# Kernel optimization log

Measured on AMD Instinct MI355X. Metric: run time of the kernel, lower is better.

The kernel has to match this reference:

```python
import jax, jax.numpy as jnp
import numpy as np

B, S, D, H = 4, 1024, 1024, 16
HD = D // H
EPS = 1e-5


def _layernorm(x, g, b):
    m = jnp.mean(x, axis=-1, keepdims=True)
    v = jnp.mean((x - m) ** 2, axis=-1, keepdims=True)
    return (x - m) * jax.lax.rsqrt(v + EPS) * g + b


def setup_inputs() -> dict:
    key = jax.random.key(0)
    ks = jax.random.split(key, 8)
    sc = 1.0 / np.sqrt(D)
    return {
        "x": jax.random.normal(ks[0], (B, S, D), dtype=jnp.float32),
        "seq_len": jax.random.randint(ks[1], (B,), 1, S + 1, dtype=jnp.int32),
        "Wq": jax.random.normal(ks[2], (D, D), dtype=jnp.float32) * sc,
        "bq": jnp.zeros((D,), dtype=jnp.float32),
        "Wk": jax.random.normal(ks[3], (D, D), dtype=jnp.float32) * sc,
        "bk": jnp.zeros((D,), dtype=jnp.float32),
        "Wv": jax.random.normal(ks[4], (D, D), dtype=jnp.float32) * sc,
        "bv": jnp.zeros((D,), dtype=jnp.float32),
        "ln_g": jnp.ones((HD,), dtype=jnp.float32),
        "ln_b": jnp.zeros((HD,), dtype=jnp.float32),
    }


def reference(x, seq_len, Wq, bq, Wk, bk, Wv, bv, ln_g, ln_b):
    # Faithful quirk: k and v are projections of the ALREADY projected q.
    q = x @ Wq.T + bq                      # [B,S,D]
    k = q @ Wk.T + bk
    v = q @ Wv.T + bv
    # [B,S,D] -> [B,H,S,HD]
    def split_heads(t):
        return t.reshape(B, S, H, HD).transpose(0, 2, 1, 3)
    q, k, v = split_heads(q), split_heads(k), split_heads(v)
    # shared per-head LayerNorm over head_dim
    q = _layernorm(q, ln_g, ln_b)
    k = _layernorm(k, ln_g, ln_b)
    v = _layernorm(v, ln_g, ln_b)
    # raw scores (no temperature scaling in the original; temperature=1.0 unused)
    scores = jnp.einsum("bhqd,bhkd->bhqk", q, k)
    # encoder_mask: multiplicative validity mask on key positions, repeated per head
    mask = (jnp.arange(S)[None, :] < seq_len[:, None]).astype(scores.dtype)  # [B,S]
    scores = scores * mask[:, None, None, :]
    attn = jax.nn.softmax(scores, axis=-1)
    # dropout is identity at inference
    out = jnp.einsum("bhqk,bhkd->bhqd", attn, v)
    return out.transpose(0, 2, 1, 3).reshape(B, S, D)
```

## Files before the change

kernel.cpp:

```cpp
#include <hip/hip_runtime.h>

#define B_  4
#define S_  1024
#define D_  1024
#define H_  16
#define HD_ 64
#define EPS_ 1e-5f

typedef _Float16 f16x8 __attribute__((ext_vector_type(8)));
typedef _Float16 f16x4 __attribute__((ext_vector_type(4)));
typedef __bf16 bf16x8 __attribute__((ext_vector_type(8)));
typedef float  f32x4  __attribute__((ext_vector_type(4)));
typedef unsigned short ushort4v __attribute__((ext_vector_type(4)));

#define GLD16(gp, lp) __builtin_amdgcn_global_load_lds( \
    (const __attribute__((address_space(1))) void*)(gp), \
    (__attribute__((address_space(3))) void*)(lp), 16, 0, 0)

static __device__ __forceinline__ unsigned pk2bf(float a, float b) {
  union { __bf16 h; unsigned short u; } ua, ub;
  ua.h = (__bf16)a; ub.h = (__bf16)b;
  return (unsigned)ua.u | ((unsigned)ub.u << 16);
}

__global__ __launch_bounds__(256) void cvt_all(
    const float* __restrict__ x,  _Float16* __restrict__ xh,
    const float* __restrict__ Wq, _Float16* __restrict__ wqh,
    const float* __restrict__ Wk, _Float16* __restrict__ wkh,
    const float* __restrict__ Wv, _Float16* __restrict__ wvh,
    float* __restrict__ Vtail) {
  int bid = blockIdx.x;
  if (bid >= 7168) {
    int i = (bid - 7168) * 1024 + threadIdx.x * 4;
    *(float4*)(Vtail + i) = make_float4(0.f, 0.f, 0.f, 0.f);
    return;
  }
  const float* src; _Float16* dst; int base;
  if (bid < 4096)      { src = x;  dst = xh;  base = bid; }
  else if (bid < 5120) { src = Wq; dst = wqh; base = bid - 4096; }
  else if (bid < 6144) { src = Wk; dst = wkh; base = bid - 5120; }
  else                 { src = Wv; dst = wvh; base = bid - 6144; }
  int i = base * 1024 + threadIdx.x * 4;
  float4 f = *(const float4*)(src + i);
  f16x4 h;
  h.x = (_Float16)f.x; h.y = (_Float16)f.y; h.z = (_Float16)f.z; h.w = (_Float16)f.w;
  *(f16x4*)(dst + i) = h;
}

__global__ __launch_bounds__(256, 2) void gemm_q_ln(
    const _Float16* __restrict__ A,
    const _Float16* __restrict__ Bw,
    const float* __restrict__ bias,
    const float* __restrict__ ln_g, const float* __restrict__ ln_b,
    _Float16* __restrict__ qh,
    _Float16* __restrict__ Qn)
{
  __shared__ _Float16 As[4 * 128 * 32];
  __shared__ _Float16 Bs[4 * 64 * 32];

  int tid  = threadIdx.x;
  int lane = tid & 63;
  int wave = tid >> 6;
  int qd = lane >> 4, l15 = lane & 15;

  int flat = blockIdx.x + 16 * blockIdx.y;
  int swz  = (flat & 7) * 64 + (flat >> 3);
  int bx = swz & 15, by = swz >> 4;

  long row0 = (long)by * 128;
  long col0 = (long)bx * 64;

  int r_a = tid >> 2;
  int c_a = (tid & 3) * 8;

  f32x4 acc[2][4] = {};

  for (int kk = 0; kk < D_; kk += 128) {
    for (int ks2 = 0; ks2 < 4; ks2++) {
      GLD16(A  + (row0 + r_a) * D_ + kk + ks2 * 32 + c_a,      As + ks2 * 4096 + tid * 8);
      GLD16(A  + (row0 + 64 + r_a) * D_ + kk + ks2 * 32 + c_a, As + ks2 * 4096 + 2048 + tid * 8);
      GLD16(Bw + (col0 + r_a) * D_ + kk + ks2 * 32 + c_a,      Bs + ks2 * 2048 + tid * 8);
    }
    __syncthreads();

    for (int ks = 0; ks < 4; ks++) {
      f16x8 af[2], bfr[4];
      for (int i = 0; i < 2; i++)
        af[i]  = *(const f16x8*)(As + ks * 4096 + (wave * 32 + i * 16 + l15) * 32 + qd * 8);
      for (int j = 0; j < 4; j++)
        bfr[j] = *(const f16x8*)(Bs + ks * 2048 + (j * 16 + l15) * 32 + qd * 8);
      for (int i = 0; i < 2; i++)
        for (int j = 0; j < 4; j++)
          acc[i][j] = __builtin_amdgcn_mfma_f32_16x16x32_f16(af[i], bfr[j], acc[i][j], 0, 0, 0);
    }
    __syncthreads();
  }

  int h = bx;
  long rw = row0 + wave * 32;
  int bb = (int)(rw >> 10);
  long bh = (long)bb * H_ + h;
  float gv[4], bl[4], bc[4];
  for (int j = 0; j < 4; j++) {
    int d = j * 16 + l15;
    gv[j] = ln_g[d]; bl[j] = ln_b[d]; bc[j] = bias[h * 64 + d];
  }
  for (int i = 0; i < 2; i++) {
    float m4[4], i4[4];
    for (int r = 0; r < 4; r++) {
      float s = 0.f, q = 0.f;
      for (int j = 0; j < 4; j++) {
        float y = acc[i][j][r] + bc[j];
        s += y; q = fmaf(y, y, q);
      }
      for (int off = 1; off < 16; off <<= 1) {
        s += __shfl_xor(s, off, 64);
        q += __shfl_xor(q, off, 64);
      }
      float m = s * (1.f / 64.f);
      m4[r] = m;
      i4[r] = rsqrtf(q * (1.f / 64.f) - m * m + EPS_);
    }
    for (int r = 0; r < 4; r++) {
      long srow = rw + i * 16 + qd * 4 + r;
      long sloc = srow & (S_ - 1);
      for (int j = 0; j < 4; j++) {
        float y = acc[i][j][r] + bc[j];
        qh[srow * D_ + h * 64 + j * 16 + l15] = (_Float16)y;
        Qn[(bh * S_ + sloc) * HD_ + j * 16 + l15] =
            (_Float16)((y - m4[r]) * i4[r] * gv[j] + bl[j]);
      }
    }
  }
}

__global__ __launch_bounds__(256, 2) void gemm_kv_ln(
    const _Float16* __restrict__ A,
    const _Float16* __restrict__ Bk, const float* __restrict__ bk,
    const _Float16* __restrict__ Bv, const float* __restrict__ bv,
    const float* __restrict__ ln_g, const float* __restrict__ ln_b,
    const int* __restrict__ seq_len,
    _Float16* __restrict__ Kn,
    unsigned short* __restrict__ Vt,
    float* __restrict__ Vtail)
{
  __shared__ _Float16 As[4 * 128 * 32];
  __shared__ _Float16 Bs[4 * 128 * 32];

  int tid  = threadIdx.x;
  int lane = tid & 63;
  int wave = tid >> 6;
  int wm = wave >> 1, wn = wave & 1;
  int qd = lane >> 4, l15 = lane & 15;

  int flat = blockIdx.x + 8 * blockIdx.y + 256 * blockIdx.z;
  int swz  = (flat & 7) * 64 + (flat >> 3);
  int z    = swz >> 8;
  int rem  = swz & 255;
  int by   = rem >> 3, bx = rem & 7;

  const _Float16* Bm = z ? Bv : Bk;
  const float* bias  = z ? bv : bk;

  long row0 = (long)by * 128;
  long col0 = (long)bx * 128;

  int r_a = tid >> 2;
  int c_a = (tid & 3) * 8;

  f32x4 acc[4][4] = {};

  for (int kk = 0; kk < D_; kk += 128) {
    for (int ks2 = 0; ks2 < 4; ks2++) {
      GLD16(A  + (row0 + r_a) * D_ + kk + ks2 * 32 + c_a,      As + ks2 * 4096 + tid * 8);
      GLD16(A  + (row0 + 64 + r_a) * D_ + kk + ks2 * 32 + c_a, As + ks2 * 4096 + 2048 + tid * 8);
      GLD16(Bm + (col0 + r_a) * D_ + kk + ks2 * 32 + c_a,      Bs + ks2 * 4096 + tid * 8);
      GLD16(Bm + (col0 + 64 + r_a) * D_ + kk + ks2 * 32 + c_a, Bs + ks2 * 4096 + 2048 + tid * 8);
    }
    __syncthreads();

    for (int ks = 0; ks < 4; ks++) {
      f16x8 af[4], bfr[4];
      for (int t = 0; t < 4; t++) {
        af[t]  = *(const f16x8*)(As + ks * 4096 + (wm * 64 + t * 16 + l15) * 32 + qd * 8);
        bfr[t] = *(const f16x8*)(Bs + ks * 4096 + (wn * 64 + t * 16 + l15) * 32 + qd * 8);
      }
      for (int i = 0; i < 4; i++)
        for (int j = 0; j < 4; j++)
          acc[i][j] = __builtin_amdgcn_mfma_f32_16x16x32_f16(af[i], bfr[j], acc[i][j], 0, 0, 0);
    }
    __syncthreads();
  }

  int h = bx * 2 + wn;
  long rw = row0 + wm * 64;
  int bb = (int)(rw >> 10);
  long bh = (long)bb * H_ + h;
  float gv[4], bl[4], bc[4];
  for (int j = 0; j < 4; j++) {
    int d = j * 16 + l15;
    gv[j] = ln_g[d]; bl[j] = ln_b[d]; bc[j] = bias[h * 64 + d];
  }

  if (z == 0) {
    for (int i = 0; i < 4; i++) {
      float m4[4], i4[4];
      for (int r = 0; r < 4; r++) {
        float s = 0.f, q = 0.f;
        for (int j = 0; j < 4; j++) {
          float y = acc[i][j][r] + bc[j];
          s += y; q = fmaf(y, y, q);
        }
        for (int off = 1; off < 16; off <<= 1) {
          s += __shfl_xor(s, off, 64);
          q += __shfl_xor(q, off, 64);
        }
        float m = s * (1.f / 64.f);
        m4[r] = m;
        i4[r] = rsqrtf(q * (1.f / 64.f) - m * m + EPS_);
      }
      for (int r = 0; r < 4; r++) {
        long sloc = (rw + i * 16 + qd * 4 + r) & (S_ - 1);
        for (int j = 0; j < 4; j++) {
          float y = acc[i][j][r] + bc[j];
          Kn[(bh * S_ + sloc) * HD_ + j * 16 + l15] =
              (_Float16)((y - m4[r]) * i4[r] * gv[j] + bl[j]);
        }
      }
    }
  } else {
    int len = seq_len[bb];
    float tsum[4] = {0.f, 0.f, 0.f, 0.f};
    for (int i = 0; i < 4; i++) {
      float m4[4], i4[4];
      for (int r = 0; r < 4; r++) {
        float s = 0.f, q = 0.f;
        for (int j = 0; j < 4; j++) {
          float y = acc[i][j][r] + bc[j];
          s += y; q = fmaf(y, y, q);
        }
        for (int off = 1; off < 16; off <<= 1) {
          s += __shfl_xor(s, off, 64);
          q += __shfl_xor(q, off, 64);
        }
        float m = s * (1.f / 64.f);
        m4[r] = m;
        i4[r] = rsqrtf(q * (1.f / 64.f) - m * m + EPS_);
      }
      int s0loc = (int)((rw + i * 16 + qd * 4) & (S_ - 1));
      for (int j = 0; j < 4; j++) {
        ushort4v w;
        for (int r = 0; r < 4; r++) {
          float y = acc[i][j][r] + bc[j];
          float vo = (y - m4[r]) * i4[r] * gv[j] + bl[j];
          __bf16 vb = (__bf16)vo;
          union { __bf16 hh; unsigned short uu; } cv; cv.hh = vb;
          w[r] = cv.uu;
          if (s0loc + r >= len) tsum[j] += (float)vb;
        }
        *(ushort4v*)(Vt + (bh * HD_ + j * 16 + l15) * S_ + s0loc) = w;
      }
    }
    if (((int)(rw & (S_ - 1)) + 64) > len)
      for (int j = 0; j < 4; j++)
        atomicAdd(&Vtail[bh * HD_ + j * 16 + l15], tsum[j]);
  }
}

__global__ __launch_bounds__(256, 4) void attn(
    const _Float16* __restrict__ Qn,
    const _Float16* __restrict__ Kn,
    const unsigned short* __restrict__ Vt,
    const float* __restrict__ Vtail,
    const int* __restrict__ seq_len,
    float* __restrict__ out)
{
  __shared__ _Float16 Ks[2][64 * 32];
  __shared__ unsigned short Vts[2][64 * 32];
  __shared__ unsigned int Pt[4][16 * 36];

  int tid = threadIdx.x, lane = tid & 63, wave = tid >> 6;
  int qd = lane >> 4, l15 = lane & 15;
  int b = blockIdx.x;
  int h = blockIdx.y;
  int q0 = blockIdx.z * 64;
  long bh = (long)b * H_ + h;
  int len = seq_len[b];
  int ntile = (len + 63) >> 6;

  int skey = tid >> 2;
  int schunk = (tid & 3) * 8;

  f16x8 qf[2];
  {
    const _Float16* qp = Qn + (bh * S_ + q0 + wave * 16 + l15) * HD_;
    qf[0] = *(const f16x8*)(qp + qd * 8);
    qf[1] = *(const f16x8*)(qp + 32 + qd * 8);
  }
  f32x4 tv[4];
  for (int t = 0; t < 4; t++)
    tv[t] = *(const f32x4*)(Vtail + bh * HD_ + t * 16 + qd * 4);

  f32x4 o[4] = {};
  float den = 0.f;

  unsigned int* pw = &Pt[wave][0];

  for (int kt = 0; kt < ntile; kt++) {
    GLD16(Kn + (bh * S_ + kt * 64 + skey) * HD_ + schunk,      &Ks[0][0] + tid * 8);
    GLD16(Kn + (bh * S_ + kt * 64 + skey) * HD_ + 32 + schunk, &Ks[1][0] + tid * 8);
    GLD16(Vt + (bh * HD_ + skey) * S_ + kt * 64 + schunk,      &Vts[0][0] + tid * 8);
    GLD16(Vt + (bh * HD_ + skey) * S_ + kt * 64 + 32 + schunk, &Vts[1][0] + tid * 8);
    __syncthreads();

    f32x4 sacc[4] = {};
    __builtin_amdgcn_s_setprio(1);
    for (int tn = 0; tn < 4; tn++) {
      f16x8 kf0 = *(const f16x8*)(&Ks[0][0] + (tn * 16 + l15) * 32 + qd * 8);
      f16x8 kf1 = *(const f16x8*)(&Ks[1][0] + (tn * 16 + l15) * 32 + qd * 8);
      sacc[tn] = __builtin_amdgcn_mfma_f32_16x16x32_f16(kf0, qf[0], sacc[tn], 0, 0, 0);
      sacc[tn] = __builtin_amdgcn_mfma_f32_16x16x32_f16(kf1, qf[1], sacc[tn], 0, 0, 0);
    }
    __builtin_amdgcn_s_setprio(0);

    if (kt * 64 + 64 <= len) {
      for (int tn = 0; tn < 4; tn++) {
        float p0 = __expf(sacc[tn][0]);
        float p1 = __expf(sacc[tn][1]);
        float p2 = __expf(sacc[tn][2]);
        float p3 = __expf(sacc[tn][3]);
        unsigned w0 = pk2bf(p0, p1);
        unsigned w1 = pk2bf(p2, p3);
        den += (float)(__bf16)p0 + (float)(__bf16)p1
             + (float)(__bf16)p2 + (float)(__bf16)p3;
        *(uint2*)(pw + l15 * 36 + tn * 8 + qd * 2) = make_uint2(w0, w1);
      }
    } else {
      for (int tn = 0; tn < 4; tn++) {
        int kg = kt * 64 + tn * 16 + qd * 4;
        float p[4];
        for (int r = 0; r < 4; r++)
          p[r] = (kg + r < len) ? __expf(sacc[tn][r]) : 0.f;
        unsigned w0 = pk2bf(p[0], p[1]);
        unsigned w1 = pk2bf(p[2], p[3]);
        den += (float)(__bf16)p[0] + (float)(__bf16)p[1]
             + (float)(__bf16)p[2] + (float)(__bf16)p[3];
        *(uint2*)(pw + l15 * 36 + tn * 8 + qd * 2) = make_uint2(w0, w1);
      }
    }

    bf16x8 pf0 = *(const bf16x8*)((const unsigned short*)pw + l15 * 72 + qd * 8);
    bf16x8 pf1 = *(const bf16x8*)((const unsigned short*)pw + l15 * 72 + 32 + qd * 8);
    __builtin_amdgcn_s_setprio(1);
    for (int t = 0; t < 4; t++) {
      bf16x8 vf0 = *(const bf16x8*)(&Vts[0][0] + (t * 16 + l15) * 32 + qd * 8);
      bf16x8 vf1 = *(const bf16x8*)(&Vts[1][0] + (t * 16 + l15) * 32 + qd * 8);
      o[t] = __builtin_amdgcn_mfma_f32_16x16x32_bf16(vf0, pf0, o[t], 0, 0, 0);
      o[t] = __builtin_amdgcn_mfma_f32_16x16x32_bf16(vf1, pf1, o[t], 0, 0, 0);
    }
    __builtin_amdgcn_s_setprio(0);
    __syncthreads();
  }

  den += __shfl_xor(den, 16, 64);
  den += __shfl_xor(den, 32, 64);
  den += (float)(S_ - len);

  long s = q0 + wave * 16 + l15;
  float* op = out + ((long)b * S_ + s) * D_ + h * 64 + qd * 4;
  for (int t = 0; t < 4; t++) {
    f32x4 r;
    for (int rr = 0; rr < 4; rr++)
      r[rr] = (o[t][rr] + tv[t][rr]) / den;
    *(f32x4*)(op + t * 16) = r;
  }
}

extern "C" void kernel_launch(void* const* d_in, const int* in_sizes, int n_in,
                              void* d_out, int out_size, void* d_ws, size_t ws_size,
                              hipStream_t stream) {
  const float* x     = (const float*)d_in[0];
  const int*  seq    = (const int*)d_in[1];
  const float* Wq    = (const float*)d_in[2];
  const float* bq    = (const float*)d_in[3];
  const float* Wk    = (const float*)d_in[4];
  const float* bk    = (const float*)d_in[5];
  const float* Wv    = (const float*)d_in[6];
  const float* bv    = (const float*)d_in[7];
  const float* ln_g  = (const float*)d_in[8];
  const float* ln_b  = (const float*)d_in[9];
  float* out = (float*)d_out;

  char* ws = (char*)d_ws;
  _Float16* xh  = (_Float16*)(ws);
  _Float16* wqh = (_Float16*)(ws + (8l  << 20));
  _Float16* wkh = (_Float16*)(ws + (10l << 20));
  _Float16* wvh = (_Float16*)(ws + (12l << 20));
  float*    Vtail = (float*)(ws + (14l << 20));
  _Float16* qh  = (_Float16*)(ws + (16l << 20));
  _Float16* Qn  = (_Float16*)(ws + (40l << 20));
  _Float16* Kn  = (_Float16*)(ws + (48l << 20));
  unsigned short* Vt = (unsigned short*)(ws + (56l << 20));

  cvt_all<<<7172, 256, 0, stream>>>(x, xh, Wq, wqh, Wk, wkh, Wv, wvh, Vtail);

  dim3 g1(D_ / 64, (B_ * S_) / 128);
  gemm_q_ln<<<g1, 256, 0, stream>>>(xh, wqh, bq, ln_g, ln_b, qh, Qn);

  dim3 g2(D_ / 128, (B_ * S_) / 128, 2);
  gemm_kv_ln<<<g2, 256, 0, stream>>>(qh, wkh, bk, wvh, bv, ln_g, ln_b, seq,
                                     Kn, Vt, Vtail);

  dim3 g4(B_, H_, S_ / 64);
  attn<<<g4, 256, 0, stream>>>(Qn, Kn, Vt, Vtail, seq, out);
}
```

Baseline: 161.3 us.

## Double-buffer LDS tiles in Q and KV projection GEMMs

Splits the shared-memory tiles into two 64-wide K stages. The next stage's global-to-LDS loads are issued before computing on the current stage, so memory latency overlaps with MFMA work in both projection GEMMs. Total LDS usage stays the same. The number of barriers per K loop doubles and each barrier has less compute to hide behind.

```diff
diff --git a/kernel.cpp b/kernel.cpp
--- a/kernel.cpp
+++ b/kernel.cpp
@@ -55,8 +55,8 @@
     _Float16* __restrict__ qh,
     _Float16* __restrict__ Qn)
 {
-  __shared__ _Float16 As[4 * 128 * 32];
-  __shared__ _Float16 Bs[4 * 64 * 32];
+  __shared__ _Float16 As[2][2 * 128 * 32];
+  __shared__ _Float16 Bs[2][2 * 64 * 32];
 
   int tid  = threadIdx.x;
   int lane = tid & 63;
@@ -75,26 +75,35 @@
 
   f32x4 acc[2][4] = {};
 
-  for (int kk = 0; kk < D_; kk += 128) {
-    for (int ks2 = 0; ks2 < 4; ks2++) {
-      GLD16(A  + (row0 + r_a) * D_ + kk + ks2 * 32 + c_a,      As + ks2 * 4096 + tid * 8);
-      GLD16(A  + (row0 + 64 + r_a) * D_ + kk + ks2 * 32 + c_a, As + ks2 * 4096 + 2048 + tid * 8);
-      GLD16(Bw + (col0 + r_a) * D_ + kk + ks2 * 32 + c_a,      Bs + ks2 * 2048 + tid * 8);
-    }
-    __syncthreads();
-
-    for (int ks = 0; ks < 4; ks++) {
+#define STAGE_Q(bf, kk) do { \
+    GLD16(A  + (row0 + r_a) * D_ + (kk) + c_a,           &As[bf][0] + tid * 8); \
+    GLD16(A  + (row0 + 64 + r_a) * D_ + (kk) + c_a,      &As[bf][0] + 2048 + tid * 8); \
+    GLD16(A  + (row0 + r_a) * D_ + (kk) + 32 + c_a,      &As[bf][0] + 4096 + tid * 8); \
+    GLD16(A  + (row0 + 64 + r_a) * D_ + (kk) + 32 + c_a, &As[bf][0] + 6144 + tid * 8); \
+    GLD16(Bw + (col0 + r_a) * D_ + (kk) + c_a,           &Bs[bf][0] + tid * 8); \
+    GLD16(Bw + (col0 + r_a) * D_ + (kk) + 32 + c_a,      &Bs[bf][0] + 2048 + tid * 8); \
+  } while (0)
+
+  STAGE_Q(0, 0);
+  __syncthreads();
+
+  for (int t = 0; t < 16; t++) {
+    int cur = t & 1;
+    if (t + 1 < 16) STAGE_Q(cur ^ 1, (t + 1) * 64);
+
+    for (int ks = 0; ks < 2; ks++) {
       f16x8 af[2], bfr[4];
       for (int i = 0; i < 2; i++)
-        af[i]  = *(const f16x8*)(As + ks * 4096 + (wave * 32 + i * 16 + l15) * 32 + qd * 8);
+        af[i]  = *(const f16x8*)(&As[cur][0] + ks * 4096 + (wave * 32 + i * 16 + l15) * 32 + qd * 8);
       for (int j = 0; j < 4; j++)
-        bfr[j] = *(const f16x8*)(Bs + ks * 2048 + (j * 16 + l15) * 32 + qd * 8);
+        bfr[j] = *(const f16x8*)(&Bs[cur][0] + ks * 2048 + (j * 16 + l15) * 32 + qd * 8);
       for (int i = 0; i < 2; i++)
         for (int j = 0; j < 4; j++)
           acc[i][j] = __builtin_amdgcn_mfma_f32_16x16x32_f16(af[i], bfr[j], acc[i][j], 0, 0, 0);
     }
     __syncthreads();
   }
+#undef STAGE_Q
 
   int h = bx;
   long rw = row0 + wave * 32;
@@ -144,8 +153,8 @@
     unsigned short* __restrict__ Vt,
     float* __restrict__ Vtail)
 {
-  __shared__ _Float16 As[4 * 128 * 32];
-  __shared__ _Float16 Bs[4 * 128 * 32];
+  __shared__ _Float16 As[2][2 * 128 * 32];
+  __shared__ _Float16 Bs[2][2 * 128 * 32];
 
   int tid  = threadIdx.x;
   int lane = tid & 63;
@@ -170,20 +179,29 @@
 
   f32x4 acc[4][4] = {};
 
-  for (int kk = 0; kk < D_; kk += 128) {
-    for (int ks2 = 0; ks2 < 4; ks2++) {
-      GLD16(A  + (row0 + r_a) * D_ + kk + ks2 * 32 + c_a,      As + ks2 * 4096 + tid * 8);
-      GLD16(A  + (row0 + 64 + r_a) * D_ + kk + ks2 * 32 + c_a, As + ks2 * 4096 + 2048 + tid * 8);
-      GLD16(Bm + (col0 + r_a) * D_ + kk + ks2 * 32 + c_a,      Bs + ks2 * 4096 + tid * 8);
-      GLD16(Bm + (col0 + 64 + r_a) * D_ + kk + ks2 * 32 + c_a, Bs + ks2 * 4096 + 2048 + tid * 8);
-    }
-    __syncthreads();
-
-    for (int ks = 0; ks < 4; ks++) {
+#define STAGE_KV(bf, kk) do { \
+    GLD16(A  + (row0 + r_a) * D_ + (kk) + c_a,           &As[bf][0] + tid * 8); \
+    GLD16(A  + (row0 + 64 + r_a) * D_ + (kk) + c_a,      &As[bf][0] + 2048 + tid * 8); \
+    GLD16(A  + (row0 + r_a) * D_ + (kk) + 32 + c_a,      &As[bf][0] + 4096 + tid * 8); \
+    GLD16(A  + (row0 + 64 + r_a) * D_ + (kk) + 32 + c_a, &As[bf][0] + 6144 + tid * 8); \
+    GLD16(Bm + (col0 + r_a) * D_ + (kk) + c_a,           &Bs[bf][0] + tid * 8); \
+    GLD16(Bm + (col0 + 64 + r_a) * D_ + (kk) + c_a,      &Bs[bf][0] + 2048 + tid * 8); \
+    GLD16(Bm + (col0 + r_a) * D_ + (kk) + 32 + c_a,      &Bs[bf][0] + 4096 + tid * 8); \
+    GLD16(Bm + (col0 + 64 + r_a) * D_ + (kk) + 32 + c_a, &Bs[bf][0] + 6144 + tid * 8); \
+  } while (0)
+
+  STAGE_KV(0, 0);
+  __syncthreads();
+
+  for (int t = 0; t < 16; t++) {
+    int cur = t & 1;
+    if (t + 1 < 16) STAGE_KV(cur ^ 1, (t + 1) * 64);
+
+    for (int ks = 0; ks < 2; ks++) {
       f16x8 af[4], bfr[4];
-      for (int t = 0; t < 4; t++) {
-        af[t]  = *(const f16x8*)(As + ks * 4096 + (wm * 64 + t * 16 + l15) * 32 + qd * 8);
-        bfr[t] = *(const f16x8*)(Bs + ks * 4096 + (wn * 64 + t * 16 + l15) * 32 + qd * 8);
+      for (int tt = 0; tt < 4; tt++) {
+        af[tt]  = *(const f16x8*)(&As[cur][0] + ks * 4096 + (wm * 64 + tt * 16 + l15) * 32 + qd * 8);
+        bfr[tt] = *(const f16x8*)(&Bs[cur][0] + ks * 4096 + (wn * 64 + tt * 16 + l15) * 32 + qd * 8);
       }
       for (int i = 0; i < 4; i++)
         for (int j = 0; j < 4; j++)
@@ -191,6 +209,7 @@
     }
     __syncthreads();
   }
+#undef STAGE_KV
 
   int h = bx * 2 + wn;
   long rw = row0 + wm * 64;
```

New measurement: 169.2 us. 4.9% more time.
